# Performance work log

Measured on AMD Instinct MI355X. Metric: run time of the kernel, lower is better.

Reference implementation:

```python
import jax, jax.numpy as jnp
import numpy as np

D_MODEL = 256
D_STATE = 128          # d_model // 2
D_CONV = 4
EXPAND = 4
D_INNER = EXPAND * D_MODEL  # 1024
DT_RANK = (D_MODEL + 15) // 16  # 16
N_HEADS = 8
D_FF = 4 * D_MODEL
EPS = 1e-6


def layer_norm(x, a, b):
    # torch LayerNorm-like but with unbiased std (ddof=1) per the source
    mean = jnp.mean(x, axis=-1, keepdims=True)
    d = x.shape[-1]
    var = jnp.sum((x - mean) ** 2, axis=-1, keepdims=True) / (d - 1)
    std = jnp.sqrt(var)
    return a * (x - mean) / (std + EPS) + b


def silu(x):
    return x * jax.nn.sigmoid(x)


def mamba(x, in_proj_w, conv_w, conv_b, x_proj_w, dt_proj_w, dt_proj_b, A_log, Dp, out_proj_w):
    B, L, _ = x.shape
    xz = jnp.einsum('bld,ed->ble', x, in_proj_w)  # (B,L,2*D_INNER)
    xi, z = xz[..., :D_INNER], xz[..., D_INNER:]
    # causal depthwise conv1d over L
    xp = jnp.pad(xi, ((0, 0), (D_CONV - 1, 0), (0, 0)))
    u = conv_b
    for k in range(D_CONV):
        u = u + xp[:, k:k + L, :] * conv_w[:, k]
    u = silu(u)  # (B,L,D_INNER)
    dbl = jnp.einsum('bld,ed->ble', u, x_proj_w)  # (B,L,DT_RANK+2*D_STATE)
    dt = dbl[..., :DT_RANK]
    Bm = dbl[..., DT_RANK:DT_RANK + D_STATE]
    Cm = dbl[..., DT_RANK + D_STATE:]
    dt = jax.nn.softplus(jnp.einsum('blr,dr->bld', dt, dt_proj_w) + dt_proj_b)  # (B,L,D_INNER)
    A = -jnp.exp(A_log)  # (D_INNER, D_STATE)
    dA = jnp.exp(jnp.einsum('bld,dn->bldn', dt, A))          # (B,L,Din,N)
    dBu = jnp.einsum('bld,bln,bld->bldn', dt, Bm, u)          # (B,L,Din,N)

    def step(h, inp):
        dA_t, dBu_t, C_t = inp
        h = dA_t * h + dBu_t                    # (B,Din,N)
        y = jnp.einsum('bdn,bn->bd', h, C_t)    # (B,Din)
        return h, y

    h0 = jnp.zeros((B, D_INNER, D_STATE), dtype=x.dtype)
    _, ys = jax.lax.scan(step, h0, (jnp.swapaxes(dA, 0, 1), jnp.swapaxes(dBu, 0, 1), jnp.swapaxes(Cm, 0, 1)))
    y = jnp.swapaxes(ys, 0, 1) + u * Dp  # (B,L,Din)
    y = y * silu(z)
    return jnp.einsum('ble,de->bld', y, out_proj_w)


def cross_attention(q_in, kv_in, mask, wq_w, wq_b, wk_w, wk_b, wv_w, wv_b, wo_w, wo_b):
    B, Lq, _ = q_in.shape
    Lk = kv_in.shape[1]
    dk = D_MODEL // N_HEADS
    q = (jnp.einsum('bld,ed->ble', q_in, wq_w) + wq_b).reshape(B, Lq, N_HEADS, dk).transpose(0, 2, 1, 3)
    k = (jnp.einsum('bld,ed->ble', kv_in, wk_w) + wk_b).reshape(B, Lk, N_HEADS, dk).transpose(0, 2, 1, 3)
    v = (jnp.einsum('bld,ed->ble', kv_in, wv_w) + wv_b).reshape(B, Lk, N_HEADS, dk).transpose(0, 2, 1, 3)
    scores = jnp.einsum('bhqd,bhkd->bhqk', q, k) / np.sqrt(dk)
    # mask: (B,1,Lk) bool -> broadcast (B,1,1,Lk)
    scores = jnp.where(mask[:, None, :, :], scores, jnp.finfo(scores.dtype).min)
    p = jax.nn.softmax(scores, axis=-1)
    o = jnp.einsum('bhqk,bhkd->bhqd', p, v).transpose(0, 2, 1, 3).reshape(B, Lq, D_MODEL)
    return jnp.einsum('ble,de->bld', o, wo_w) + wo_b


def setup_inputs() -> dict:
    key = jax.random.key(0)
    ks = jax.random.split(key, 24)
    s = 0.02
    B, L, Lm = 2, 512, 512
    inp = {
        'x': jax.random.normal(ks[0], (B, L, D_MODEL), jnp.float32),
        'memory': jax.random.normal(ks[1], (B, Lm, D_MODEL), jnp.float32),
        'src_mask': jnp.ones((B, 1, Lm), bool),
        'tgt_mask': jnp.ones((B, 1, L), bool),
        # mamba params
        'in_proj_w': jax.random.normal(ks[2], (2 * D_INNER, D_MODEL)) * s,
        'conv_w': jax.random.normal(ks[3], (D_INNER, D_CONV)) * s,
        'conv_b': jnp.zeros((D_INNER,)),
        'x_proj_w': jax.random.normal(ks[4], (DT_RANK + 2 * D_STATE, D_INNER)) * s,
        'dt_proj_w': jax.random.normal(ks[5], (D_INNER, DT_RANK)) * s,
        'dt_proj_b': jnp.log(jnp.expm1(0.01)) * jnp.ones((D_INNER,)),
        'A_log': jnp.log(jnp.broadcast_to(jnp.arange(1, D_STATE + 1, dtype=jnp.float32), (D_INNER, D_STATE))),
        'Dp': jnp.ones((D_INNER,)),
        'out_proj_w': jax.random.normal(ks[6], (D_MODEL, D_INNER)) * s,
        # norms
        'norm1_a': jnp.ones((D_MODEL,)), 'norm1_b': jnp.zeros((D_MODEL,)),
        'norm2_a': jnp.ones((D_MODEL,)), 'norm2_b': jnp.zeros((D_MODEL,)),
        'norm3_a': jnp.ones((D_MODEL,)), 'norm3_b': jnp.zeros((D_MODEL,)),
        # cross attention
        'wq_w': jax.random.normal(ks[7], (D_MODEL, D_MODEL)) * s, 'wq_b': jnp.zeros((D_MODEL,)),
        'wk_w': jax.random.normal(ks[8], (D_MODEL, D_MODEL)) * s, 'wk_b': jnp.zeros((D_MODEL,)),
        'wv_w': jax.random.normal(ks[9], (D_MODEL, D_MODEL)) * s, 'wv_b': jnp.zeros((D_MODEL,)),
        'wo_w': jax.random.normal(ks[10], (D_MODEL, D_MODEL)) * s, 'wo_b': jnp.zeros((D_MODEL,)),
        # ffn
        'w1_w': jax.random.normal(ks[11], (D_FF, D_MODEL)) * s, 'w1_b': jnp.zeros((D_FF,)),
        'w2_w': jax.random.normal(ks[12], (D_MODEL, D_FF)) * s, 'w2_b': jnp.zeros((D_MODEL,)),
    }
    return inp


def reference(x, memory, src_mask, tgt_mask,
              in_proj_w, conv_w, conv_b, x_proj_w, dt_proj_w, dt_proj_b, A_log, Dp, out_proj_w,
              norm1_a, norm1_b, norm2_a, norm2_b, norm3_a, norm3_b,
              wq_w, wq_b, wk_w, wk_b, wv_w, wv_b, wo_w, wo_b,
              w1_w, w1_b, w2_w, w2_b):
    # self mamba block (pre-norm, residual); dropout = 0
    h = x + mamba(layer_norm(x, norm1_a, norm1_b), in_proj_w, conv_w, conv_b,
                  x_proj_w, dt_proj_w, dt_proj_b, A_log, Dp, out_proj_w)
    # cross attention block
    h = h + cross_attention(layer_norm(h, norm2_a, norm2_b), memory, src_mask,
                            wq_w, wq_b, wk_w, wk_b, wv_w, wv_b, wo_w, wo_b)
    # ffn block
    hn = layer_norm(h, norm3_a, norm3_b)
    ff = jnp.einsum('blf,df->bld', jax.nn.relu(jnp.einsum('bld,fd->blf', hn, w1_w) + w1_b), w2_w) + w2_b
    return h + ff
```

## Files before the change

### kernel.cpp

```cpp
#include <hip/hip_runtime.h>
#include <hip/hip_bf16.h>

#define B_SZ 2
#define L_SEQ 512
#define D_MODEL 256
#define D_STATE 128
#define D_CONV 4
#define D_INNER 1024
#define DT_RANK 16
#define N_HEADS 8
#define DK 32
#define D_FF 1024
#define R_TOT (B_SZ * L_SEQ)
#define DBL_LD (DT_RANK + 2 * D_STATE)
#define NSEG 16
#define SEGL 32

typedef __hip_bfloat16 bf16;
typedef __attribute__((ext_vector_type(8))) short short8;
typedef __attribute__((ext_vector_type(4))) float floatx4;

__device__ inline float fexp(float x) { return __expf(x); }
__device__ inline float frcp(float x) { return __builtin_amdgcn_rcpf(x); }
__device__ inline float silu_f(float x) { return x * frcp(1.f + fexp(-x)); }
__device__ inline float softplus_f(float x) { return (x > 20.f) ? x : __logf(1.f + fexp(x)); }

__device__ inline float dpp_sum64(float x) {
    x += __int_as_float(__builtin_amdgcn_update_dpp(0, __float_as_int(x), 0x111, 0xf, 0xf, true));
    x += __int_as_float(__builtin_amdgcn_update_dpp(0, __float_as_int(x), 0x112, 0xf, 0xf, true));
    x += __int_as_float(__builtin_amdgcn_update_dpp(0, __float_as_int(x), 0x114, 0xf, 0xf, true));
    x += __int_as_float(__builtin_amdgcn_update_dpp(0, __float_as_int(x), 0x118, 0xf, 0xf, true));
    x += __int_as_float(__builtin_amdgcn_update_dpp(0, __float_as_int(x), 0x142, 0xf, 0xf, true));
    x += __int_as_float(__builtin_amdgcn_update_dpp(0, __float_as_int(x), 0x143, 0xf, 0xf, true));
    return x;
}

#define S_MEM 262144
#define S_INW 524288
#define S_XPW 278528
#define S_OPW 262144
#define S_WQ  65536
#define S_WK  65536
#define S_WV  65536
#define S_WO  65536
#define S_W1  262144
#define S_W2  262144
#define S_TOT (S_MEM+S_INW+S_XPW+S_OPW+S_WQ+S_WK+S_WV+S_WO+S_W1+S_W2)
#define PACK_BLKS ((S_TOT + 255) / 256)
#define Z1_F4 (4 * R_TOT * D_MODEL / 4)
#define Z2_F4 (R_TOT * D_MODEL / 4)
#define Z3_F4 (R_TOT * DBL_LD / 4)
#define ZERO_BLKS ((Z1_F4 + Z2_F4 + Z3_F4 + 255) / 256)

__global__ __launch_bounds__(256) void pack_ln1(
    const float* __restrict__ s0, const float* __restrict__ s1,
    const float* __restrict__ s2, const float* __restrict__ s3,
    const float* __restrict__ s4, const float* __restrict__ s5,
    const float* __restrict__ s6, const float* __restrict__ s7,
    const float* __restrict__ s8, const float* __restrict__ s9,
    bf16* __restrict__ dst,
    const float* __restrict__ X, const float* __restrict__ a,
    const float* __restrict__ bvec, bf16* __restrict__ ln1b,
    float* __restrict__ zero1, float* __restrict__ zero2,
    float* __restrict__ zero3)
{
    __shared__ float r1[256], r2[256];
    if (blockIdx.x < PACK_BLKS) {
        const long i = (long)blockIdx.x * 256 + threadIdx.x;
        if (i >= S_TOT) return;
        const long off[11] = {0, S_MEM, S_MEM+S_INW, S_MEM+S_INW+S_XPW,
            S_MEM+S_INW+S_XPW+S_OPW, S_MEM+S_INW+S_XPW+S_OPW+S_WQ,
            S_MEM+S_INW+S_XPW+S_OPW+S_WQ+S_WK,
            S_MEM+S_INW+S_XPW+S_OPW+S_WQ+S_WK+S_WV,
            S_MEM+S_INW+S_XPW+S_OPW+S_WQ+S_WK+S_WV+S_WO,
            S_MEM+S_INW+S_XPW+S_OPW+S_WQ+S_WK+S_WV+S_WO+S_W1, S_TOT};
        const float* srcs[10] = {s0,s1,s2,s3,s4,s5,s6,s7,s8,s9};
        int seg = 0;
#pragma unroll
        for (int k = 1; k < 10; ++k) if (i >= off[k]) seg = k;
        dst[i] = __float2bfloat16(srcs[seg][i - off[seg]]);
    } else if (blockIdx.x < PACK_BLKS + R_TOT) {
        const int row = blockIdx.x - PACK_BLKS;
        const int t = threadIdx.x;
        const float v = X[(long)row * D_MODEL + t];
        r1[t] = v;
        r2[t] = v * v;
        __syncthreads();
        for (int s = 128; s > 0; s >>= 1) {
            if (t < s) { r1[t] += r1[t + s]; r2[t] += r2[t + s]; }
            __syncthreads();
        }
        const float mean = r1[0] * (1.f / 256.f);
        const float var = (r2[0] - 256.f * mean * mean) * (1.f / 255.f);
        const float sd = sqrtf(fmaxf(var, 0.f));
        const float o = a[t] * (v - mean) / (sd + 1e-6f) + bvec[t];
        ln1b[(long)row * D_MODEL + t] = __float2bfloat16(o);
    } else {
        const long i4 = (long)(blockIdx.x - PACK_BLKS - R_TOT) * 256 + threadIdx.x;
        const float4 z = {0.f, 0.f, 0.f, 0.f};
        if (i4 < Z1_F4)                      *(float4*)&zero1[i4 * 4] = z;
        else if (i4 < Z1_F4 + Z2_F4)          *(float4*)&zero2[(i4 - Z1_F4) * 4] = z;
        else if (i4 < Z1_F4 + Z2_F4 + Z3_F4)  *(float4*)&zero3[(i4 - Z1_F4 - Z2_F4) * 4] = z;
    }
}

template <int EPI>
__global__ __launch_bounds__(256) void mfma_gemm(
    const bf16* __restrict__ A, const bf16* __restrict__ W, int K,
    float* __restrict__ C, bf16* __restrict__ Cb, int ldc,
    const float* __restrict__ bias, const float* __restrict__ res,
    int M, int N)
{
    const int wave = threadIdx.x >> 6;
    const int lane = threadIdx.x & 63;
    const int row16 = lane & 15;
    const int quad  = lane >> 4;
    const int bm = blockIdx.y * 64 + wave * 16;
    const int bn = blockIdx.x * 64;

    floatx4 acc[4];
#pragma unroll
    for (int t = 0; t < 4; ++t) acc[t] = (floatx4){0.f, 0.f, 0.f, 0.f};

    const long arow = (long)(bm + row16) * K;
    for (int k0 = 0; k0 < K; k0 += 32) {
        const short8 av = *(const short8*)(A + arow + k0 + quad * 8);
#pragma unroll
        for (int t = 0; t < 4; ++t) {
            const int gn = bn + t * 16 + row16;
            short8 bv = {0,0,0,0,0,0,0,0};
            if (gn < N) bv = *(const short8*)(W + (long)gn * K + k0 + quad * 8);
            acc[t] = __builtin_amdgcn_mfma_f32_16x16x32_bf16(av, bv, acc[t], 0, 0, 0);
        }
    }

#pragma unroll
    for (int t = 0; t < 4; ++t) {
        const int gn = bn + t * 16 + row16;
        if (gn >= N) continue;
        const float bs = bias ? bias[gn] : 0.f;
#pragma unroll
        for (int r = 0; r < 4; ++r) {
            const int gm = bm + quad * 4 + r;
            float v = acc[t][r] + bs;
            if (EPI == 1) v = fmaxf(v, 0.f);
            const long ci = (long)gm * ldc + gn;
            if (res) v += res[ci];
            if (C)  C[ci] = v;
            if (Cb) Cb[ci] = __float2bfloat16(v);
        }
    }
}

template <int SK>
__global__ __launch_bounds__(256) void splitk_gemm(
    const bf16* __restrict__ A, const bf16* __restrict__ W, int K,
    float* __restrict__ C, int ldc,
    const float* __restrict__ bias, const float* __restrict__ res,
    int M, int N)
{
    const int wave = threadIdx.x >> 6;
    const int lane = threadIdx.x & 63;
    const int row16 = lane & 15;
    const int quad  = lane >> 4;
    const int bm = blockIdx.y * 64 + wave * 16;
    const int bn = blockIdx.x * 64;
    const int kz = blockIdx.z;
    const int ksl = K / SK;
    const int kbeg = kz * ksl;

    floatx4 acc[4];
#pragma unroll
    for (int t = 0; t < 4; ++t) acc[t] = (floatx4){0.f, 0.f, 0.f, 0.f};

    const long arow = (long)(bm + row16) * K;
    for (int k0 = kbeg; k0 < kbeg + ksl; k0 += 32) {
        const short8 av = *(const short8*)(A + arow + k0 + quad * 8);
#pragma unroll
        for (int t = 0; t < 4; ++t) {
            const int gn = bn + t * 16 + row16;
            short8 bv = {0,0,0,0,0,0,0,0};
            if (gn < N) bv = *(const short8*)(W + (long)gn * K + k0 + quad * 8);
            acc[t] = __builtin_amdgcn_mfma_f32_16x16x32_bf16(av, bv, acc[t], 0, 0, 0);
        }
    }

#pragma unroll
    for (int t = 0; t < 4; ++t) {
        const int gn = bn + t * 16 + row16;
        if (gn >= N) continue;
        const float bs = (kz == 0 && bias) ? bias[gn] : 0.f;
#pragma unroll
        for (int r = 0; r < 4; ++r) {
            const int gm = bm + quad * 4 + r;
            float v = acc[t][r] + bs;
            const long ci = (long)gm * ldc + gn;
            if (kz == 0 && res) v += res[ci];
            atomicAdd(&C[ci], v);
        }
    }
}

__global__ __launch_bounds__(256) void gemm16_ln(
    const bf16* __restrict__ A, const bf16* __restrict__ W, int K,
    const float* __restrict__ bias, const float* __restrict__ res,
    float* __restrict__ Cf,
    const float* __restrict__ lna, const float* __restrict__ lnb,
    bf16* __restrict__ lnout)
{
    __shared__ float tile[16][264];
    __shared__ float red1[16][16];
    __shared__ float red2[16][16];
    const int w = threadIdx.x >> 6;
    const int lane = threadIdx.x & 63;
    const int row16 = lane & 15;
    const int quad  = lane >> 4;
    const int bm = blockIdx.x * 16;

    floatx4 acc[4];
#pragma unroll
    for (int t = 0; t < 4; ++t) acc[t] = (floatx4){0.f, 0.f, 0.f, 0.f};

    const long arow = (long)(bm + row16) * K;
    for (int k0 = 0; k0 < K; k0 += 32) {
        const short8 av = *(const short8*)(A + arow + k0 + quad * 8);
#pragma unroll
        for (int t = 0; t < 4; ++t) {
            const int gn = w * 64 + t * 16 + row16;
            const short8 bv = *(const short8*)(W + (long)gn * K + k0 + quad * 8);
            acc[t] = __builtin_amdgcn_mfma_f32_16x16x32_bf16(av, bv, acc[t], 0, 0, 0);
        }
    }

#pragma unroll
    for (int t = 0; t < 4; ++t) {
        const int gn = w * 64 + t * 16 + row16;
        const float bs = bias ? bias[gn] : 0.f;
#pragma unroll
        for (int r = 0; r < 4; ++r) {
            const int gm = bm + quad * 4 + r;
            float v = acc[t][r] + bs;
            const long ci = (long)gm * D_MODEL + gn;
            if (res) v += res[ci];
            Cf[ci] = v;
            tile[quad * 4 + r][gn] = v;
        }
    }
    __syncthreads();

    const int r = threadIdx.x >> 4;
    const int g = threadIdx.x & 15;
    float s = 0.f, q = 0.f;
#pragma unroll
    for (int i = 0; i < 16; ++i) {
        const float x = tile[r][g * 16 + i];
        s += x; q += x * x;
    }
    red1[r][g] = s; red2[r][g] = q;
    __syncthreads();
    float ts = 0.f, tq = 0.f;
#pragma unroll
    for (int i = 0; i < 16; ++i) { ts += red1[r][i]; tq += red2[r][i]; }
    const float mean = ts * (1.f / 256.f);
    const float var = (tq - 256.f * mean * mean) * (1.f / 255.f);
    const float sd = sqrtf(fmaxf(var, 0.f));
    const long rowbase = (long)(bm + r) * D_MODEL;
#pragma unroll
    for (int i = 0; i < 16; ++i) {
        const int c = g * 16 + i;
        const float o = lna[c] * (tile[r][c] - mean) / (sd + 1e-6f) + lnb[c];
        lnout[rowbase + c] = __float2bfloat16(o);
    }
}

__global__ __launch_bounds__(256) void ln_kernel(
    const float* __restrict__ x, const float* __restrict__ a,
    const float* __restrict__ bvec, bf16* __restrict__ out)
{
    const int row = blockIdx.x;
    const int t = threadIdx.x;
    const float v = x[(long)row * D_MODEL + t];
    __shared__ float r1[256], r2[256];
    r1[t] = v;
    r2[t] = v * v;
    __syncthreads();
    for (int s = 128; s > 0; s >>= 1) {
        if (t < s) { r1[t] += r1[t + s]; r2[t] += r2[t + s]; }
        __syncthreads();
    }
    const float mean = r1[0] * (1.f / 256.f);
    const float var = (r2[0] - 256.f * mean * mean) * (1.f / 255.f);
    const float sd = sqrtf(fmaxf(var, 0.f));
    const float o = a[t] * (v - mean) / (sd + 1e-6f) + bvec[t];
    out[(long)row * D_MODEL + t] = __float2bfloat16(o);
}

__global__ __launch_bounds__(256) void qkv_gemm(
    const bf16* __restrict__ ln2b, const bf16* __restrict__ memb,
    const bf16* __restrict__ WQb, const bf16* __restrict__ WKb,
    const bf16* __restrict__ WVb,
    const float* __restrict__ WQB, const float* __restrict__ WKB,
    const float* __restrict__ WVB,
    float* __restrict__ qb, float* __restrict__ kb, float* __restrict__ vb)
{
    const int which = blockIdx.z >> 1;
    const int kz = blockIdx.z & 1;
    const bf16* A = (which == 0) ? ln2b : memb;
    const bf16* W = (which == 0) ? WQb : (which == 1) ? WKb : WVb;
    const float* bias = (which == 0) ? WQB : (which == 1) ? WKB : WVB;
    float* C = (which == 0) ? qb : (which == 1) ? kb : vb;

    const int wave = threadIdx.x >> 6;
    const int lane = threadIdx.x & 63;
    const int row16 = lane & 15;
    const int quad  = lane >> 4;
    const int bm = blockIdx.y * 64 + wave * 16;
    const int bn = blockIdx.x * 64;
    const int kbeg = kz * (D_MODEL / 2);

    floatx4 acc[4];
#pragma unroll
    for (int t = 0; t < 4; ++t) acc[t] = (floatx4){0.f, 0.f, 0.f, 0.f};

    const long arow = (long)(bm + row16) * D_MODEL;
    for (int k0 = kbeg; k0 < kbeg + D_MODEL / 2; k0 += 32) {
        const short8 av = *(const short8*)(A + arow + k0 + quad * 8);
#pragma unroll
        for (int t = 0; t < 4; ++t) {
            const int gn = bn + t * 16 + row16;
            const short8 bv = *(const short8*)(W + (long)gn * D_MODEL + k0 + quad * 8);
            acc[t] = __builtin_amdgcn_mfma_f32_16x16x32_bf16(av, bv, acc[t], 0, 0, 0);
        }
    }
#pragma unroll
    for (int t = 0; t < 4; ++t) {
        const int gn = bn + t * 16 + row16;
        const float bs = (kz == 0) ? bias[gn] : 0.f;
#pragma unroll
        for (int r = 0; r < 4; ++r) {
            const int gm = bm + quad * 4 + r;
            atomicAdd(&C[(long)gm * D_MODEL + gn], acc[t][r] + bs);
        }
    }
}

__global__ __launch_bounds__(256) void dt_gemm_T(
    const float* __restrict__ A , const float* __restrict__ W ,
    const float* __restrict__ bias, float* __restrict__ dtT)
{
    __shared__ float As[DT_RANK][65];
    __shared__ float Bs[DT_RANK][65];
    __shared__ float Ct[64][65];
    const int bm = blockIdx.y * 64;
    const int bn = blockIdx.x * 64;
    const int tid = threadIdx.x;
    const int tx = tid & 15;
    const int ty = tid >> 4;
    const int r = tid >> 2;
    const int kk = (tid & 3) * 4;
#pragma unroll
    for (int q = 0; q < 4; ++q) {
        As[kk + q][r] = A[(long)(bm + r) * DBL_LD + kk + q];
        Bs[kk + q][r] = W[(long)(bn + r) * DT_RANK + kk + q];
    }
    __syncthreads();
    float acc[4][4] = {};
#pragma unroll
    for (int k = 0; k < DT_RANK; ++k) {
        float a[4], bv[4];
#pragma unroll
        for (int i = 0; i < 4; ++i) a[i] = As[k][ty * 4 + i];
#pragma unroll
        for (int j = 0; j < 4; ++j) bv[j] = Bs[k][tx * 4 + j];
#pragma unroll
        for (int i = 0; i < 4; ++i)
#pragma unroll
            for (int j = 0; j < 4; ++j)
                acc[i][j] = fmaf(a[i], bv[j], acc[i][j]);
    }
#pragma unroll
    for (int i = 0; i < 4; ++i)
#pragma unroll
        for (int j = 0; j < 4; ++j)
            Ct[tx * 4 + j][ty * 4 + i] = softplus_f(acc[i][j] + bias[bn + tx * 4 + j]);
    __syncthreads();
    const int b = bm >> 9;
    const int l0 = bm & 511;
    const int r2 = tid >> 4;
    const int c4 = (tid & 15) * 4;
#pragma unroll
    for (int q = 0; q < 4; ++q) {
        const int dl = r2 + q * 16;
        float4 v = {Ct[dl][c4], Ct[dl][c4 + 1], Ct[dl][c4 + 2], Ct[dl][c4 + 3]};
        *(float4*)&dtT[((long)(b * D_INNER + bn + dl) << 9) + l0 + c4] = v;
    }
}

__global__ __launch_bounds__(256) void conv_silu_T(
    const float* __restrict__ xz, const float* __restrict__ cw,
    const float* __restrict__ cb, bf16* __restrict__ ub, float* __restrict__ uT)
{
    __shared__ float t[64][65];
    const int db = blockIdx.x;
    const int lb = blockIdx.y;
    const int b  = blockIdx.z;
    const int tid = threadIdx.x;
    const int r  = tid >> 4;
    const int c4 = (tid & 15) * 4;
    const int d0 = db * 64 + c4;

    const float4 cb4 = *(const float4*)&cb[d0];
    float cwa[4][4];
#pragma unroll
    for (int i = 0; i < 4; ++i) {
        const float4 w = *(const float4*)&cw[(d0 + i) * 4];
        cwa[i][0] = w.x; cwa[i][1] = w.y; cwa[i][2] = w.z; cwa[i][3] = w.w;
    }

#pragma unroll
    for (int q = 0; q < 4; ++q) {
        const int ll = r + q * 16;
        const int l = lb * 64 + ll;
        float s0 = cb4.x, s1 = cb4.y, s2 = cb4.z, s3 = cb4.w;
#pragma unroll
        for (int k = 0; k < D_CONV; ++k) {
            const int ls = l - 3 + k;
            if (ls >= 0) {
                const float4 xv = *(const float4*)&xz[((long)(b * L_SEQ + ls)) * (2 * D_INNER) + d0];
                s0 = fmaf(xv.x, cwa[0][k], s0);
                s1 = fmaf(xv.y, cwa[1][k], s1);
                s2 = fmaf(xv.z, cwa[2][k], s2);
                s3 = fmaf(xv.w, cwa[3][k], s3);
            }
        }
        s0 = silu_f(s0); s1 = silu_f(s1); s2 = silu_f(s2); s3 = silu_f(s3);
        bf16 b0 = __float2bfloat16(s0), b1 = __float2bfloat16(s1);
        bf16 b2 = __float2bfloat16(s2), b3 = __float2bfloat16(s3);
        ushort4 pk;
        pk.x = *reinterpret_cast<unsigned short*>(&b0);
        pk.y = *reinterpret_cast<unsigned short*>(&b1);
        pk.z = *reinterpret_cast<unsigned short*>(&b2);
        pk.w = *reinterpret_cast<unsigned short*>(&b3);
        *reinterpret_cast<ushort4*>(ub + ((long)(b * L_SEQ + l)) * D_INNER + d0) = pk;
        t[c4 + 0][ll] = s0; t[c4 + 1][ll] = s1;
        t[c4 + 2][ll] = s2; t[c4 + 3][ll] = s3;
    }
    __syncthreads();
#pragma unroll
    for (int q = 0; q < 4; ++q) {
        const int dl = r + q * 16;
        float4 v = {t[dl][c4], t[dl][c4 + 1], t[dl][c4 + 2], t[dl][c4 + 3]};
        *(float4*)&uT[((long)(b * D_INNER + db * 64 + dl) << 9) + lb * 64 + c4] = v;
    }
}

__global__ __launch_bounds__(1024) void scan_fused(
    const float* __restrict__ dtT, const float* __restrict__ uT,
    const float* __restrict__ dbl, const float* __restrict__ A_log,
    float* __restrict__ ysT)
{
    const int cd = blockIdx.x;
    const int b = cd >> 10;
    const int d = cd & 1023;
    const int w = threadIdx.x >> 6;
    const int lane = threadIdx.x & 63;
    const int n0 = lane * 2;

    __shared__ float Sh[NSEG][D_STATE];
    __shared__ float Ph[NSEG][D_STATE];

    const float An0 = -fexp(A_log[(long)d * D_STATE + n0]);
    const float An1 = -fexp(A_log[(long)d * D_STATE + n0 + 1]);

    const float* dtp = dtT + ((long)cd << 9) + w * SEGL;
    const float* up  = uT  + ((long)cd << 9) + w * SEGL;
    const float* blp = dbl + ((long)(b * L_SEQ + w * SEGL)) * DBL_LD + DT_RANK + n0;
    const float* clp = blp + D_STATE;

    if (w < NSEG - 1) {
        float h0 = 0.f, h1 = 0.f, sdt = 0.f;
        for (int s = 0; s < SEGL / 8; ++s) {
            const float4 dt0 = *(const float4*)(dtp + s * 8);
            const float4 dt1 = *(const float4*)(dtp + s * 8 + 4);
            const float4 u0  = *(const float4*)(up + s * 8);
            const float4 u1  = *(const float4*)(up + s * 8 + 4);
            float2 Bv[8];
#pragma unroll
            for (int j = 0; j < 8; ++j)
                Bv[j] = *(const float2*)(blp + (long)(s * 8 + j) * DBL_LD);
            const float dts[8] = {dt0.x, dt0.y, dt0.z, dt0.w, dt1.x, dt1.y, dt1.z, dt1.w};
            const float us[8]  = {u0.x,  u0.y,  u0.z,  u0.w,  u1.x,  u1.y,  u1.z,  u1.w};
#pragma unroll
            for (int j = 0; j < 8; ++j) {
                const float dtv = dts[j];
                sdt += dtv;
                const float dtu = dtv * us[j];
                h0 = fmaf(fexp(dtv * An0), h0, dtu * Bv[j].x);
                h1 = fmaf(fexp(dtv * An1), h1, dtu * Bv[j].y);
            }
        }
        Sh[w][n0] = h0; Sh[w][n0 + 1] = h1;
        Ph[w][n0] = fexp(An0 * sdt); Ph[w][n0 + 1] = fexp(An1 * sdt);
    }
    __syncthreads();

    float h0 = 0.f, h1 = 0.f;
    for (int s = 0; s < w; ++s) {
        h0 = fmaf(Ph[s][n0],     h0, Sh[s][n0]);
        h1 = fmaf(Ph[s][n0 + 1], h1, Sh[s][n0 + 1]);
    }

    float* ysp = ysT + ((long)cd << 9) + w * SEGL;
    for (int s = 0; s < SEGL / 8; ++s) {
        const float4 dt0 = *(const float4*)(dtp + s * 8);
        const float4 dt1 = *(const float4*)(dtp + s * 8 + 4);
        const float4 u0  = *(const float4*)(up + s * 8);
        const float4 u1  = *(const float4*)(up + s * 8 + 4);
        float2 Bv[8], Cv[8];
#pragma unroll
        for (int j = 0; j < 8; ++j) {
            Bv[j] = *(const float2*)(blp + (long)(s * 8 + j) * DBL_LD);
            Cv[j] = *(const float2*)(clp + (long)(s * 8 + j) * DBL_LD);
        }
        const float dts[8] = {dt0.x, dt0.y, dt0.z, dt0.w, dt1.x, dt1.y, dt1.z, dt1.w};
        const float us[8]  = {u0.x,  u0.y,  u0.z,  u0.w,  u1.x,  u1.y,  u1.z,  u1.w};
        float yp[8];
#pragma unroll
        for (int j = 0; j < 8; ++j) {
            const float dtv = dts[j];
            const float dtu = dtv * us[j];
            h0 = fmaf(fexp(dtv * An0), h0, dtu * Bv[j].x);
            h1 = fmaf(fexp(dtv * An1), h1, dtu * Bv[j].y);
            yp[j] = fmaf(h0, Cv[j].x, h1 * Cv[j].y);
        }
#pragma unroll
        for (int j = 0; j < 8; ++j) yp[j] = dpp_sum64(yp[j]);

        if (lane == 63) {
            *(float4*)(ysp + s * 8)     = (float4){yp[0], yp[1], yp[2], yp[3]};
            *(float4*)(ysp + s * 8 + 4) = (float4){yp[4], yp[5], yp[6], yp[7]};
        }
    }
}

__global__ __launch_bounds__(256) void gate_kernel(
    const float* __restrict__ ysT, const float* __restrict__ uT,
    const float* __restrict__ Dp, const float* __restrict__ xz,
    bf16* __restrict__ y)
{
    __shared__ float t[64][65];
    __shared__ float t2[64][65];
    const int db = blockIdx.x;
    const int lb = blockIdx.y;
    const int b  = blockIdx.z;
    const int tid = threadIdx.x;
    const int r  = tid >> 4;
    const int c4 = (tid & 15) * 4;

#pragma unroll
    for (int q = 0; q < 4; ++q) {
        const int dr = r + q * 16;
        const long base = (((long)(b * D_INNER + db * 64 + dr)) << 9) + lb * 64 + c4;
        const float4 v = *(const float4*)&ysT[base];
        const float4 w = *(const float4*)&uT[base];
        t[dr][c4 + 0] = v.x; t[dr][c4 + 1] = v.y;
        t[dr][c4 + 2] = v.z; t[dr][c4 + 3] = v.w;
        t2[dr][c4 + 0] = w.x; t2[dr][c4 + 1] = w.y;
        t2[dr][c4 + 2] = w.z; t2[dr][c4 + 3] = w.w;
    }
    __syncthreads();

    const float4 dp4 = *(const float4*)&Dp[db * 64 + c4];
#pragma unroll
    for (int q = 0; q < 4; ++q) {
        const int lr = r + q * 16;
        const long row = (long)b * L_SEQ + lb * 64 + lr;
        const float4 z4 = *(const float4*)&xz[row * 2 * D_INNER + D_INNER + db * 64 + c4];
        const float r0 = (t[c4 + 0][lr] + t2[c4 + 0][lr] * dp4.x) * silu_f(z4.x);
        const float r1 = (t[c4 + 1][lr] + t2[c4 + 1][lr] * dp4.y) * silu_f(z4.y);
        const float r2 = (t[c4 + 2][lr] + t2[c4 + 2][lr] * dp4.z) * silu_f(z4.z);
        const float r3 = (t[c4 + 3][lr] + t2[c4 + 3][lr] * dp4.w) * silu_f(z4.w);
        bf16 b0 = __float2bfloat16(r0), b1 = __float2bfloat16(r1);
        bf16 b2 = __float2bfloat16(r2), b3 = __float2bfloat16(r3);
        ushort4 pk;
        pk.x = *reinterpret_cast<unsigned short*>(&b0);
        pk.y = *reinterpret_cast<unsigned short*>(&b1);
        pk.z = *reinterpret_cast<unsigned short*>(&b2);
        pk.w = *reinterpret_cast<unsigned short*>(&b3);
        *reinterpret_cast<ushort4*>(y + row * D_INNER + db * 64 + c4) = pk;
    }
}

#define QT 16
#define CK 64

__global__ __launch_bounds__(256) void attn_kernel(
    const float* __restrict__ q, const float* __restrict__ k,
    const float* __restrict__ v, bf16* __restrict__ o)
{
    const int qt = blockIdx.x;
    const int hh = blockIdx.y;
    const int b  = blockIdx.z;
    const int t = threadIdx.x;
    const int lane = t & 15;
    const int qa = t >> 4;
    const int q0 = qt * QT + qa;

    __shared__ float Ks[CK][36];
    __shared__ float Vs[CK][36];

    const float scale = 0.17677669529663687f;
    float qr0[32];
    {
        const float* q0p = q + ((long)(b * L_SEQ + q0) * D_MODEL + hh * DK);
#pragma unroll
        for (int i = 0; i < 8; ++i) {
            const float4 a = *(const float4*)&q0p[i * 4];
            qr0[i*4+0] = a.x * scale; qr0[i*4+1] = a.y * scale;
            qr0[i*4+2] = a.z * scale; qr0[i*4+3] = a.w * scale;
        }
    }

    float m0 = -1e30f, l0 = 0.f, o0[32] = {};

    for (int c = 0; c < L_SEQ; c += CK) {
        __syncthreads();
        {
            const int fid = t * 2;
            const int row = fid >> 3;
            const int c0  = (fid & 7) * 4;
            const float* kp = k + ((long)(b * L_SEQ + c + row) * D_MODEL + hh * DK + c0);
            const float* vp = v + ((long)(b * L_SEQ + c + row) * D_MODEL + hh * DK + c0);
            *(float4*)&Ks[row][c0]     = *(const float4*)kp;
            *(float4*)&Ks[row][c0 + 4] = *(const float4*)(kp + 4);
            *(float4*)&Vs[row][c0]     = *(const float4*)vp;
            *(float4*)&Vs[row][c0 + 4] = *(const float4*)(vp + 4);
        }
        __syncthreads();

        float s0[4];
#pragma unroll
        for (int i = 0; i < 4; ++i) {
            const int kk = i * 16 + lane;
            float a0 = 0.f;
#pragma unroll
            for (int dd = 0; dd < 32; dd += 4) {
                const float4 kv = *(const float4*)&Ks[kk][dd];
                a0 = fmaf(qr0[dd+0], kv.x, a0); a0 = fmaf(qr0[dd+1], kv.y, a0);
                a0 = fmaf(qr0[dd+2], kv.z, a0); a0 = fmaf(qr0[dd+3], kv.w, a0);
            }
            s0[i] = a0;
        }

        float cm0 = s0[0];
#pragma unroll
        for (int i = 1; i < 4; ++i) cm0 = fmaxf(cm0, s0[i]);
#pragma unroll
        for (int off = 8; off > 0; off >>= 1)
            cm0 = fmaxf(cm0, __shfl_down(cm0, off, 16));
        cm0 = __shfl(cm0, 0, 16);

        const float nm0 = fmaxf(m0, cm0);
        const float al0 = fexp(m0 - nm0);
        l0 *= al0;
#pragma unroll
        for (int dd = 0; dd < 32; ++dd) o0[dd] *= al0;
        m0 = nm0;

        float p0[4];
#pragma unroll
        for (int i = 0; i < 4; ++i) { p0[i] = fexp(s0[i] - m0); l0 += p0[i]; }

#pragma unroll
        for (int i = 0; i < 4; ++i) {
            const int kk = i * 16 + lane;
#pragma unroll
            for (int dd = 0; dd < 32; dd += 4) {
                const float4 vv = *(const float4*)&Vs[kk][dd];
                o0[dd+0] = fmaf(p0[i], vv.x, o0[dd+0]);
                o0[dd+1] = fmaf(p0[i], vv.y, o0[dd+1]);
                o0[dd+2] = fmaf(p0[i], vv.z, o0[dd+2]);
                o0[dd+3] = fmaf(p0[i], vv.w, o0[dd+3]);
            }
        }
    }

#pragma unroll
    for (int off = 8; off > 0; off >>= 1) {
        l0 += __shfl_down(l0, off, 16);
#pragma unroll
        for (int dd = 0; dd < 32; ++dd) o0[dd] += __shfl_down(o0[dd], off, 16);
    }
    if (lane == 0) {
        const float i0 = 1.f / l0;
        bf16* op0 = o + ((long)(b * L_SEQ + q0) * D_MODEL + hh * DK);
#pragma unroll
        for (int dd = 0; dd < 32; ++dd) op0[dd] = __float2bfloat16(o0[dd] * i0);
    }
}


extern "C" void kernel_launch(void* const* d_in, const int* in_sizes, int n_in,
                              void* d_out, int out_size, void* d_ws, size_t ws_size,
                              hipStream_t stream) {
    const float* X   = (const float*)d_in[0];
    const float* MEM = (const float*)d_in[1];
    const float* CW  = (const float*)d_in[5];
    const float* CB  = (const float*)d_in[6];
    const float* DTW = (const float*)d_in[8];
    const float* DTB = (const float*)d_in[9];
    const float* ALG = (const float*)d_in[10];
    const float* DP  = (const float*)d_in[11];
    const float* N1A = (const float*)d_in[13];
    const float* N1B = (const float*)d_in[14];
    const float* N2A = (const float*)d_in[15];
    const float* N2B = (const float*)d_in[16];
    const float* N3A = (const float*)d_in[17];
    const float* N3B = (const float*)d_in[18];
    const float* WQB = (const float*)d_in[20];
    const float* WKB = (const float*)d_in[22];
    const float* WVB = (const float*)d_in[24];
    const float* WOB = (const float*)d_in[26];
    const float* W1B = (const float*)d_in[28];
    const float* W2B = (const float*)d_in[30];
    const float* INW = (const float*)d_in[4];
    const float* XPW = (const float*)d_in[7];
    const float* OPW = (const float*)d_in[12];
    const float* WQ  = (const float*)d_in[19];
    const float* WKw = (const float*)d_in[21];
    const float* WVw = (const float*)d_in[23];
    const float* WO  = (const float*)d_in[25];
    const float* W1  = (const float*)d_in[27];
    const float* W2  = (const float*)d_in[29];
    float* out = (float*)d_out;

    bf16* bp = (bf16*)d_ws;
    bf16* ub   = bp;  bp += (long)R_TOT * D_INNER;
    bf16* ybb  = bp;  bp += (long)R_TOT * D_INNER;
    bf16* ffab = ybb;
    bf16* ln1b = bp;  bp += (long)R_TOT * D_MODEL;
    bf16* aob  = ln1b;
    bf16* ln2b = bp;  bp += (long)R_TOT * D_MODEL;
    bf16* ln3b = ln2b;
    bf16* arena = bp; bp += S_TOT;
    bf16* MEMb = arena;
    bf16* INWb = MEMb + S_MEM;
    bf16* XPWb = INWb + S_INW;
    bf16* OPWb = XPWb + S_XPW;
    bf16* WQb  = OPWb + S_OPW;
    bf16* WKb  = WQb + S_WQ;
    bf16* WVb  = WKb + S_WK;
    bf16* WOb  = WVb + S_WV;
    bf16* W1b  = WOb + S_WO;
    bf16* W2b  = W1b + S_W1;

    float* p = (float*)(bp + ((((long)(bp - (bf16*)d_ws)) & 1) ? 1 : 0));
    float* xz  = p;                                  p += (long)R_TOT * 2 * D_INNER;
    float* uT  = p;                                  p += (long)R_TOT * D_INNER;
    float* dbl = p;                                  p += (long)R_TOT * DBL_LD;
    float* dtT = p;                                  p += (long)R_TOT * D_INNER;
    float* ysT = p;                                  p += (long)R_TOT * D_INNER;
    float* h1  = p;                                  p += (long)R_TOT * D_MODEL;
    float* qb  = p;                                  p += (long)R_TOT * D_MODEL;
    float* kb  = p;                                  p += (long)R_TOT * D_MODEL;
    float* vb  = p;                                  p += (long)R_TOT * D_MODEL;
    float* h2  = p;                                  p += (long)R_TOT * D_MODEL;

    const dim3 blk256(256);
    const int MT64 = R_TOT / 64;

    pack_ln1<<<PACK_BLKS + R_TOT + ZERO_BLKS, blk256, 0, stream>>>(
        MEM, INW, XPW, OPW, WQ, WKw, WVw, WO, W1, W2, arena,
        X, N1A, N1B, ln1b, h1, out, dbl);

    mfma_gemm<0><<<dim3(2 * D_INNER / 64, MT64), blk256, 0, stream>>>(
        ln1b, INWb, D_MODEL, xz, nullptr, 2 * D_INNER, nullptr, nullptr,
        R_TOT, 2 * D_INNER);

    conv_silu_T<<<dim3(D_INNER / 64, L_SEQ / 64, B_SZ), blk256, 0, stream>>>(
        xz, CW, CB, ub, uT);

    splitk_gemm<4><<<dim3((DBL_LD + 63) / 64, MT64, 4), blk256, 0, stream>>>(
        ub, XPWb, D_INNER, dbl, DBL_LD, nullptr, nullptr, R_TOT, DBL_LD);

    dt_gemm_T<<<dim3(D_INNER / 64, MT64), blk256, 0, stream>>>(dbl, DTW, DTB, dtT);

    scan_fused<<<B_SZ * D_INNER, dim3(1024), 0, stream>>>(dtT, uT, dbl, ALG, ysT);

    gate_kernel<<<dim3(D_INNER / 64, L_SEQ / 64, B_SZ), blk256, 0, stream>>>(
        ysT, uT, DP, xz, ybb);

    splitk_gemm<4><<<dim3(D_MODEL / 64, MT64, 4), blk256, 0, stream>>>(
        ybb, OPWb, D_INNER, h1, D_MODEL, nullptr, X, R_TOT, D_MODEL);

    ln_kernel<<<R_TOT, blk256, 0, stream>>>(h1, N2A, N2B, ln2b);

    qkv_gemm<<<dim3(D_MODEL / 64, MT64, 6), blk256, 0, stream>>>(
        ln2b, MEMb, WQb, WKb, WVb, WQB, WKB, WVB, qb, kb, vb);

    attn_kernel<<<dim3(L_SEQ / QT, N_HEADS, B_SZ), blk256, 0, stream>>>(qb, kb, vb, aob);

    gemm16_ln<<<R_TOT / 16, blk256, 0, stream>>>(
        aob, WOb, D_MODEL, WOB, h1, h2, N3A, N3B, ln3b);

    mfma_gemm<1><<<dim3(D_FF / 64, MT64), blk256, 0, stream>>>(
        ln3b, W1b, D_MODEL, nullptr, ffab, D_FF, W1B, nullptr, R_TOT, D_FF);

    splitk_gemm<4><<<dim3(D_MODEL / 64, MT64, 4), blk256, 0, stream>>>(
        ffab, W2b, D_FF, out, D_MODEL, W2B, h2, R_TOT, D_MODEL);

    (void)in_sizes; (void)n_in; (void)out_size; (void)ws_size;
}
```

Before: 381.2 us.

## Store xz in bf16 and fuse K/V projection into x_proj GEMM launch

```diff
diff --git a/kernel.cpp b/kernel.cpp
--- a/kernel.cpp
+++ b/kernel.cpp
@@ -24,6 +24,7 @@
 __device__ inline float frcp(float x) { return __builtin_amdgcn_rcpf(x); }
 __device__ inline float silu_f(float x) { return x * frcp(1.f + fexp(-x)); }
 __device__ inline float softplus_f(float x) { return (x > 20.f) ? x : __logf(1.f + fexp(x)); }
+__device__ inline float bf2f(unsigned short u) { return __uint_as_float(((unsigned)u) << 16); }
 
 __device__ inline float dpp_sum64(float x) {
     x += __int_as_float(__builtin_amdgcn_update_dpp(0, __float_as_int(x), 0x111, 0xf, 0xf, true));
@@ -201,6 +202,108 @@
     }
 }
 
+__global__ __launch_bounds__(256) void xproj_kv_gemm(
+    const bf16* __restrict__ ub, const bf16* __restrict__ XPWb,
+    float* __restrict__ dbl,
+    const bf16* __restrict__ memb, const bf16* __restrict__ WKb,
+    const bf16* __restrict__ WVb,
+    const float* __restrict__ WKB, const float* __restrict__ WVB,
+    float* __restrict__ kb, float* __restrict__ vb)
+{
+    const int wave = threadIdx.x >> 6;
+    const int lane = threadIdx.x & 63;
+    const int row16 = lane & 15;
+    const int quad  = lane >> 4;
+    const int bm = blockIdx.y * 64 + wave * 16;
+    const int bn = blockIdx.x * 64;
+    const int z = blockIdx.z;
+
+    const bf16* A; const bf16* W; const float* bias; float* C;
+    int K, N, ldc, kbeg, ksl;
+    if (z < 4) {
+        A = ub; W = XPWb; bias = nullptr; C = dbl;
+        K = D_INNER; N = DBL_LD; ldc = DBL_LD;
+        ksl = D_INNER / 4; kbeg = z * ksl;
+    } else {
+        if (bn >= D_MODEL) return;
+        const int zz = z - 4;
+        const int which = zz >> 1;
+        const int kz = zz & 1;
+        A = memb; W = which ? WVb : WKb;
+        bias = (kz == 0) ? (which ? WVB : WKB) : nullptr;
+        C = which ? vb : kb;
+        K = D_MODEL; N = D_MODEL; ldc = D_MODEL;
+        ksl = D_MODEL / 2; kbeg = kz * ksl;
+    }
+
+    floatx4 acc[4];
+#pragma unroll
+    for (int t = 0; t < 4; ++t) acc[t] = (floatx4){0.f, 0.f, 0.f, 0.f};
+
+    const long arow = (long)(bm + row16) * K;
+    for (int k0 = kbeg; k0 < kbeg + ksl; k0 += 32) {
+        const short8 av = *(const short8*)(A + arow + k0 + quad * 8);
+#pragma unroll
+        for (int t = 0; t < 4; ++t) {
+            const int gn = bn + t * 16 + row16;
+            short8 bv = {0,0,0,0,0,0,0,0};
+            if (gn < N) bv = *(const short8*)(W + (long)gn * K + k0 + quad * 8);
+            acc[t] = __builtin_amdgcn_mfma_f32_16x16x32_bf16(av, bv, acc[t], 0, 0, 0);
+        }
+    }
+
+#pragma unroll
+    for (int t = 0; t < 4; ++t) {
+        const int gn = bn + t * 16 + row16;
+        if (gn >= N) continue;
+        const float bs = bias ? bias[gn] : 0.f;
+#pragma unroll
+        for (int r = 0; r < 4; ++r) {
+            const int gm = bm + quad * 4 + r;
+            atomicAdd(&C[(long)gm * ldc + gn], acc[t][r] + bs);
+        }
+    }
+}
+
+__global__ __launch_bounds__(256) void q_gemm(
+    const bf16* __restrict__ ln2b, const bf16* __restrict__ WQb,
+    const float* __restrict__ WQB, float* __restrict__ qb)
+{
+    const int wave = threadIdx.x >> 6;
+    const int lane = threadIdx.x & 63;
+    const int row16 = lane & 15;
+    const int quad  = lane >> 4;
+    const int bm = blockIdx.y * 64 + wave * 16;
+    const int bn = blockIdx.x * 64;
+    const int kz = blockIdx.z;
+    const int kbeg = kz * (D_MODEL / 2);
+
+    floatx4 acc[4];
+#pragma unroll
+    for (int t = 0; t < 4; ++t) acc[t] = (floatx4){0.f, 0.f, 0.f, 0.f};
+
+    const long arow = (long)(bm + row16) * D_MODEL;
+    for (int k0 = kbeg; k0 < kbeg + D_MODEL / 2; k0 += 32) {
+        const short8 av = *(const short8*)(ln2b + arow + k0 + quad * 8);
+#pragma unroll
+        for (int t = 0; t < 4; ++t) {
+            const int gn = bn + t * 16 + row16;
+            const short8 bv = *(const short8*)(WQb + (long)gn * D_MODEL + k0 + quad * 8);
+            acc[t] = __builtin_amdgcn_mfma_f32_16x16x32_bf16(av, bv, acc[t], 0, 0, 0);
+        }
+    }
+#pragma unroll
+    for (int t = 0; t < 4; ++t) {
+        const int gn = bn + t * 16 + row16;
+        const float bs = (kz == 0) ? WQB[gn] : 0.f;
+#pragma unroll
+        for (int r = 0; r < 4; ++r) {
+            const int gm = bm + quad * 4 + r;
+            atomicAdd(&qb[(long)gm * D_MODEL + gn], acc[t][r] + bs);
+        }
+    }
+}
+
 __global__ __launch_bounds__(256) void gemm16_ln(
     const bf16* __restrict__ A, const bf16* __restrict__ W, int K,
     const float* __restrict__ bias, const float* __restrict__ res,
@@ -295,55 +398,6 @@
     out[(long)row * D_MODEL + t] = __float2bfloat16(o);
 }
 
-__global__ __launch_bounds__(256) void qkv_gemm(
-    const bf16* __restrict__ ln2b, const bf16* __restrict__ memb,
-    const bf16* __restrict__ WQb, const bf16* __restrict__ WKb,
-    const bf16* __restrict__ WVb,
-    const float* __restrict__ WQB, const float* __restrict__ WKB,
-    const float* __restrict__ WVB,
-    float* __restrict__ qb, float* __restrict__ kb, float* __restrict__ vb)
-{
-    const int which = blockIdx.z >> 1;
-    const int kz = blockIdx.z & 1;
-    const bf16* A = (which == 0) ? ln2b : memb;
-    const bf16* W = (which == 0) ? WQb : (which == 1) ? WKb : WVb;
-    const float* bias = (which == 0) ? WQB : (which == 1) ? WKB : WVB;
-    float* C = (which == 0) ? qb : (which == 1) ? kb : vb;
-
-    const int wave = threadIdx.x >> 6;
-    const int lane = threadIdx.x & 63;
-    const int row16 = lane & 15;
-    const int quad  = lane >> 4;
-    const int bm = blockIdx.y * 64 + wave * 16;
-    const int bn = blockIdx.x * 64;
-    const int kbeg = kz * (D_MODEL / 2);
-
-    floatx4 acc[4];
-#pragma unroll
-    for (int t = 0; t < 4; ++t) acc[t] = (floatx4){0.f, 0.f, 0.f, 0.f};
-
-    const long arow = (long)(bm + row16) * D_MODEL;
-    for (int k0 = kbeg; k0 < kbeg + D_MODEL / 2; k0 += 32) {
-        const short8 av = *(const short8*)(A + arow + k0 + quad * 8);
-#pragma unroll
-        for (int t = 0; t < 4; ++t) {
-            const int gn = bn + t * 16 + row16;
-            const short8 bv = *(const short8*)(W + (long)gn * D_MODEL + k0 + quad * 8);
-            acc[t] = __builtin_amdgcn_mfma_f32_16x16x32_bf16(av, bv, acc[t], 0, 0, 0);
-        }
-    }
-#pragma unroll
-    for (int t = 0; t < 4; ++t) {
-        const int gn = bn + t * 16 + row16;
-        const float bs = (kz == 0) ? bias[gn] : 0.f;
-#pragma unroll
-        for (int r = 0; r < 4; ++r) {
-            const int gm = bm + quad * 4 + r;
-            atomicAdd(&C[(long)gm * D_MODEL + gn], acc[t][r] + bs);
-        }
-    }
-}
-
 __global__ __launch_bounds__(256) void dt_gemm_T(
     const float* __restrict__ A , const float* __restrict__ W ,
     const float* __restrict__ bias, float* __restrict__ dtT)
@@ -397,7 +451,7 @@
 }
 
 __global__ __launch_bounds__(256) void conv_silu_T(
-    const float* __restrict__ xz, const float* __restrict__ cw,
+    const bf16* __restrict__ xz, const float* __restrict__ cw,
     const float* __restrict__ cb, bf16* __restrict__ ub, float* __restrict__ uT)
 {
     __shared__ float t[64][65];
@@ -426,11 +480,11 @@
         for (int k = 0; k < D_CONV; ++k) {
             const int ls = l - 3 + k;
             if (ls >= 0) {
-                const float4 xv = *(const float4*)&xz[((long)(b * L_SEQ + ls)) * (2 * D_INNER) + d0];
-                s0 = fmaf(xv.x, cwa[0][k], s0);
-                s1 = fmaf(xv.y, cwa[1][k], s1);
-                s2 = fmaf(xv.z, cwa[2][k], s2);
-                s3 = fmaf(xv.w, cwa[3][k], s3);
+                const ushort4 xv = *(const ushort4*)&xz[((long)(b * L_SEQ + ls)) * (2 * D_INNER) + d0];
+                s0 = fmaf(bf2f(xv.x), cwa[0][k], s0);
+                s1 = fmaf(bf2f(xv.y), cwa[1][k], s1);
+                s2 = fmaf(bf2f(xv.z), cwa[2][k], s2);
+                s3 = fmaf(bf2f(xv.w), cwa[3][k], s3);
             }
         }
         s0 = silu_f(s0); s1 = silu_f(s1); s2 = silu_f(s2); s3 = silu_f(s3);
@@ -545,7 +599,7 @@
 
 __global__ __launch_bounds__(256) void gate_kernel(
     const float* __restrict__ ysT, const float* __restrict__ uT,
-    const float* __restrict__ Dp, const float* __restrict__ xz,
+    const float* __restrict__ Dp, const bf16* __restrict__ xz,
     bf16* __restrict__ y)
 {
     __shared__ float t[64][65];
@@ -575,11 +629,11 @@
     for (int q = 0; q < 4; ++q) {
         const int lr = r + q * 16;
         const long row = (long)b * L_SEQ + lb * 64 + lr;
-        const float4 z4 = *(const float4*)&xz[row * 2 * D_INNER + D_INNER + db * 64 + c4];
-        const float r0 = (t[c4 + 0][lr] + t2[c4 + 0][lr] * dp4.x) * silu_f(z4.x);
-        const float r1 = (t[c4 + 1][lr] + t2[c4 + 1][lr] * dp4.y) * silu_f(z4.y);
-        const float r2 = (t[c4 + 2][lr] + t2[c4 + 2][lr] * dp4.z) * silu_f(z4.z);
-        const float r3 = (t[c4 + 3][lr] + t2[c4 + 3][lr] * dp4.w) * silu_f(z4.w);
+        const ushort4 zu = *(const ushort4*)&xz[row * 2 * D_INNER + D_INNER + db * 64 + c4];
+        const float r0 = (t[c4 + 0][lr] + t2[c4 + 0][lr] * dp4.x) * silu_f(bf2f(zu.x));
+        const float r1 = (t[c4 + 1][lr] + t2[c4 + 1][lr] * dp4.y) * silu_f(bf2f(zu.y));
+        const float r2 = (t[c4 + 2][lr] + t2[c4 + 2][lr] * dp4.z) * silu_f(bf2f(zu.z));
+        const float r3 = (t[c4 + 3][lr] + t2[c4 + 3][lr] * dp4.w) * silu_f(bf2f(zu.w));
         bf16 b0 = __float2bfloat16(r0), b1 = __float2bfloat16(r1);
         bf16 b2 = __float2bfloat16(r2), b3 = __float2bfloat16(r3);
         ushort4 pk;
@@ -738,6 +792,7 @@
     bf16* ub   = bp;  bp += (long)R_TOT * D_INNER;
     bf16* ybb  = bp;  bp += (long)R_TOT * D_INNER;
     bf16* ffab = ybb;
+    bf16* xzb  = bp;  bp += (long)R_TOT * 2 * D_INNER;
     bf16* ln1b = bp;  bp += (long)R_TOT * D_MODEL;
     bf16* aob  = ln1b;
     bf16* ln2b = bp;  bp += (long)R_TOT * D_MODEL;
@@ -755,7 +810,6 @@
     bf16* W2b  = W1b + S_W1;
 
     float* p = (float*)(bp + ((((long)(bp - (bf16*)d_ws)) & 1) ? 1 : 0));
-    float* xz  = p;                                  p += (long)R_TOT * 2 * D_INNER;
     float* uT  = p;                                  p += (long)R_TOT * D_INNER;
     float* dbl = p;                                  p += (long)R_TOT * DBL_LD;
     float* dtT = p;                                  p += (long)R_TOT * D_INNER;
@@ -774,29 +828,28 @@
         X, N1A, N1B, ln1b, h1, out, dbl);
 
     mfma_gemm<0><<<dim3(2 * D_INNER / 64, MT64), blk256, 0, stream>>>(
-        ln1b, INWb, D_MODEL, xz, nullptr, 2 * D_INNER, nullptr, nullptr,
+        ln1b, INWb, D_MODEL, nullptr, xzb, 2 * D_INNER, nullptr, nullptr,
         R_TOT, 2 * D_INNER);
 
     conv_silu_T<<<dim3(D_INNER / 64, L_SEQ / 64, B_SZ), blk256, 0, stream>>>(
-        xz, CW, CB, ub, uT);
-
-    splitk_gemm<4><<<dim3((DBL_LD + 63) / 64, MT64, 4), blk256, 0, stream>>>(
-        ub, XPWb, D_INNER, dbl, DBL_LD, nullptr, nullptr, R_TOT, DBL_LD);
+        xzb, CW, CB, ub, uT);
+
+    xproj_kv_gemm<<<dim3((DBL_LD + 63) / 64, MT64, 8), blk256, 0, stream>>>(
+        ub, XPWb, dbl, MEMb, WKb, WVb, WKB, WVB, kb, vb);
 
     dt_gemm_T<<<dim3(D_INNER / 64, MT64), blk256, 0, stream>>>(dbl, DTW, DTB, dtT);
 
     scan_fused<<<B_SZ * D_INNER, dim3(1024), 0, stream>>>(dtT, uT, dbl, ALG, ysT);
 
     gate_kernel<<<dim3(D_INNER / 64, L_SEQ / 64, B_SZ), blk256, 0, stream>>>(
-        ysT, uT, DP, xz, ybb);
+        ysT, uT, DP, xzb, ybb);
 
     splitk_gemm<4><<<dim3(D_MODEL / 64, MT64, 4), blk256, 0, stream>>>(
         ybb, OPWb, D_INNER, h1, D_MODEL, nullptr, X, R_TOT, D_MODEL);
 
     ln_kernel<<<R_TOT, blk256, 0, stream>>>(h1, N2A, N2B, ln2b);
 
-    qkv_gemm<<<dim3(D_MODEL / 64, MT64, 6), blk256, 0, stream>>>(
-        ln2b, MEMb, WQb, WKb, WVb, WQB, WKB, WVB, qb, kb, vb);
+    q_gemm<<<dim3(D_MODEL / 64, MT64, 2), blk256, 0, stream>>>(ln2b, WQb, WQB, qb);
 
     attn_kernel<<<dim3(L_SEQ / QT, N_HEADS, B_SZ), blk256, 0, stream>>>(qb, kb, vb, aob);
 
```

Measured after the change: 379.2 us. About the same (-0.5%).
